# Kernel tuning notes

Hardware: AMD Instinct MI355X
Metric: run time of the kernel (lower is better)

Reference implementation:

```python
import jax, jax.numpy as jnp
import numpy as np

N_T, N_M, E, Q = 100000, 20000, 600000, 200000
F_IN, D, L = 256, 128, 2


def setup_inputs() -> dict:
    key = jax.random.key(0)
    ks = jax.random.split(key, 20)
    s = 1.0 / np.sqrt(D)
    inp = {
        "x_thesis": jax.random.normal(ks[0], (N_T, F_IN), jnp.float32),
        "mentor_node_id": jnp.arange(N_M, dtype=jnp.int64) if jax.config.jax_enable_x64 else jnp.arange(N_M, dtype=jnp.int32),
        "edge_src": jax.random.randint(ks[1], (E,), 0, N_T),
        "edge_dst": jax.random.randint(ks[2], (E,), 0, N_M),
        "eli_src": jax.random.randint(ks[3], (Q,), 0, N_T),
        "eli_dst": jax.random.randint(ks[4], (Q,), 0, N_M),
        # encoder params
        "thesis_lin_w": jax.random.normal(ks[5], (D, F_IN), jnp.float32) / np.sqrt(F_IN),
        "thesis_lin_b": jnp.zeros((D,), jnp.float32),
        "prof_emb": jax.random.normal(ks[6], (N_M, D), jnp.float32),
        # SAGEConv params per layer, per edge type (sup: thesis->mentor, rev: mentor->thesis)
        "W_nbr_sup": jax.random.normal(ks[7], (L, D, D), jnp.float32) * s,
        "W_root_sup": jax.random.normal(ks[8], (L, D, D), jnp.float32) * s,
        "b_sup": jnp.zeros((L, D), jnp.float32),
        "W_nbr_rev": jax.random.normal(ks[9], (L, D, D), jnp.float32) * s,
        "W_root_rev": jax.random.normal(ks[10], (L, D, D), jnp.float32) * s,
        "b_rev": jnp.zeros((L, D), jnp.float32),
        # classifier Linear(2*D -> 1)
        "cls_w": jax.random.normal(ks[11], (2 * D,), jnp.float32) * (1.0 / np.sqrt(2 * D)),
        "cls_b": jnp.zeros((), jnp.float32),
    }
    return inp


def reference(x_thesis, mentor_node_id, edge_src, edge_dst, eli_src, eli_dst,
              thesis_lin_w, thesis_lin_b, prof_emb,
              W_nbr_sup, W_root_sup, b_sup, W_nbr_rev, W_root_rev, b_rev,
              cls_w, cls_b):
    n_t = x_thesis.shape[0]
    n_m = prof_emb.shape[0]
    L_ = W_nbr_sup.shape[0]

    # node encoders
    h_t = x_thesis @ thesis_lin_w.T + thesis_lin_b          # [N_T, D]
    h_m = prof_emb[mentor_node_id]                          # [N_M, D]

    ones = jnp.ones(edge_src.shape[0], h_t.dtype)
    deg_m = jnp.maximum(jax.ops.segment_sum(ones, edge_dst, num_segments=n_m), 1.0)[:, None]
    deg_t = jnp.maximum(jax.ops.segment_sum(ones, edge_src, num_segments=n_t), 1.0)[:, None]

    for l in range(L_):
        # mean-aggregate thesis feats onto mentors (supervised_by edges)
        agg_m = jax.ops.segment_sum(h_t[edge_src], edge_dst, num_segments=n_m) / deg_m
        # mean-aggregate mentor feats onto theses (reverse edges)
        agg_t = jax.ops.segment_sum(h_m[edge_dst], edge_src, num_segments=n_t) / deg_t
        new_m = agg_m @ W_nbr_sup[l].T + h_m @ W_root_sup[l].T + b_sup[l]
        new_t = agg_t @ W_nbr_rev[l].T + h_t @ W_root_rev[l].T + b_rev[l]
        if l < L_ - 1:
            new_m = jax.nn.relu(new_m)
            new_t = jax.nn.relu(new_t)
        h_t, h_m = new_t, new_m

    # edge-level classifier: gather endpoints, concat, linear -> scalar per pair
    z = jnp.concatenate([h_t[eli_src], h_m[eli_dst]], axis=-1)  # [Q, 2D]
    return z @ cls_w + cls_b                                     # [Q]
```

## Files before the change

kernel.cpp:

```cpp
#include <hip/hip_runtime.h>
#include <cstdint>
#include <cstddef>

#define D 128
#define F_IN 256

typedef __attribute__((ext_vector_type(8))) short bf16x8;
typedef __attribute__((ext_vector_type(4))) float f32x4;

__device__ __forceinline__ unsigned short f2bs(float f) {
  unsigned int x = __builtin_bit_cast(unsigned int, f);
  x = x + 0x7fffu + ((x >> 16) & 1u);
  return (unsigned short)(x >> 16);
}
__device__ __forceinline__ unsigned pk2(float lo, float hi) {
  return (unsigned)f2bs(lo) | ((unsigned)f2bs(hi) << 16);
}
__device__ __forceinline__ float b2f(unsigned int lo16) {
  unsigned int x = lo16 << 16;
  return __builtin_bit_cast(float, x);
}
__device__ __forceinline__ void gl_lds16v(const void* g, void* l) {
  __builtin_amdgcn_global_load_lds(
      (__attribute__((address_space(1))) void*)g,
      (__attribute__((address_space(3))) void*)l, 16, 0, 0);
}
__device__ __forceinline__ uint4 pack8(float4 a, float4 b) {
  uint4 o;
  o.x = pk2(a.x, a.y); o.y = pk2(a.z, a.w);
  o.z = pk2(b.x, b.y); o.w = pk2(b.z, b.w);
  return o;
}


__global__ __launch_bounds__(256) void prep_k(
    const float* __restrict__ s0, unsigned short* __restrict__ d0, int n0,
    const float* __restrict__ s1, unsigned short* __restrict__ d1, int n1,
    const float* __restrict__ s2, unsigned short* __restrict__ d2, int n2,
    const float* __restrict__ s3, unsigned short* __restrict__ d3, int n3,
    const float* __restrict__ s4, unsigned short* __restrict__ d4, int n4,
    int nbC,
    const float* __restrict__ emb, const int* __restrict__ ids,
    unsigned short* __restrict__ hm, int NM, int nbG,
    const int* __restrict__ esrc, const int* __restrict__ edst,
    int* __restrict__ bktT, int* __restrict__ bktM,
    int E, int SHT, int SHM, int nbA)
{
  int bid = blockIdx.x;
  int tid = threadIdx.x;
  if (bid < nbC) {
    int j = bid * 256 + tid;
    const float* s; unsigned short* d;
    if (j < n0) { s = s0; d = d0; }
    else {
      j -= n0;
      if (j < n1) { s = s1; d = d1; }
      else {
        j -= n1;
        if (j < n2) { s = s2; d = d2; }
        else {
          j -= n2;
          if (j < n3) { s = s3; d = d3; }
          else { j -= n3; if (j >= n4) return; s = s4; d = d4; }
        }
      }
    }
    const float4* sp = (const float4*)(s + (size_t)j * 8);
    *(uint4*)(d + (size_t)j * 8) = pack8(sp[0], sp[1]);
    return;
  }
  bid -= nbC;
  if (bid < nbG) {
    int i = bid * 256 + tid;
    if (i >= NM * 16) return;
    int r = i >> 4, c = (i & 15) * 8;
    const float* s = emb + (size_t)ids[r] * D + c;
    *(uint4*)(hm + (size_t)r * D + c) = pack8(*(const float4*)s, *(const float4*)(s + 4));
    return;
  }
  bid -= nbG;
  __shared__ int sh[256];
  sh[tid] = 0;
  __syncthreads();
  int stride = nbA * 256;
  for (int e = bid * 256 + tid; e < E; e += stride) {
    atomicAdd(&sh[esrc[e] >> SHT], 1);
    atomicAdd(&sh[128 + (edst[e] >> SHM)], 1);
  }
  __syncthreads();
  if (tid < 128) { if (sh[tid]) atomicAdd(&bktT[tid], sh[tid]); }
  else { if (sh[tid]) atomicAdd(&bktM[tid - 128], sh[tid]); }
}


__global__ void a2_scan_k(const int* __restrict__ bktT, int* __restrict__ baseT, int* __restrict__ curT, int BT,
                          const int* __restrict__ bktM, int* __restrict__ baseM, int* __restrict__ curM, int BM) {
  __shared__ int sT[129], sM[129];
  int tid = threadIdx.x;
  if (tid < BT) sT[tid] = bktT[tid];
  if (tid < BM) sM[tid] = bktM[tid];
  __syncthreads();
  if (tid == 0) { int r = 0; for (int i = 0; i < BT; ++i) { int c = sT[i]; sT[i] = r; r += c; } sT[BT] = r; }
  if (tid == 1) { int r = 0; for (int i = 0; i < BM; ++i) { int c = sM[i]; sM[i] = r; r += c; } sM[BM] = r; }
  __syncthreads();
  if (tid <= BT) { baseT[tid] = sT[tid]; if (tid < BT) curT[tid] = sT[tid]; }
  if (tid <= BM) { baseM[tid] = sM[tid]; if (tid < BM) curM[tid] = sM[tid]; }
}


#define CH 4096

__global__ __launch_bounds__(256) void a3_part_k(
    const int* __restrict__ esrc, const int* __restrict__ edst,
    unsigned* __restrict__ partT, unsigned* __restrict__ partM,
    int* __restrict__ curT, int* __restrict__ curM,
    int E, int BT, int BM, int SHT, int SHM)
{
  __shared__ unsigned stT[CH], stM[CH];
  __shared__ int hT[128], lbT[128], lcT[128], gbT[128];
  __shared__ int hM[128], lbM[128], lcM[128], gbM[128];
  __shared__ int st2[256];
  int tid = threadIdx.x;
  int c0 = blockIdx.x * CH;
  int len = E - c0; if (len > CH) len = CH;

  if (tid < 128) { hT[tid] = 0; hM[tid] = 0; }
  __syncthreads();
  for (int i = tid; i < len; i += 256) {
    atomicAdd(&hT[esrc[c0 + i] >> SHT], 1);
    atomicAdd(&hM[edst[c0 + i] >> SHM], 1);
  }
  __syncthreads();
  int own = (tid < 128) ? hT[tid] : hM[tid - 128];
  st2[tid] = own;
  __syncthreads();
  for (int dd = 1; dd < 128; dd <<= 1) {
    int y = ((tid & 127) >= dd) ? st2[tid - dd] : 0;
    __syncthreads();
    st2[tid] += y;
    __syncthreads();
  }
  int excl = st2[tid] - own;
  if (tid < 128) { lbT[tid] = excl; lcT[tid] = excl; }
  else { lbM[tid - 128] = excl; lcM[tid - 128] = excl; }
  __syncthreads();
  if (tid < BT) { if (hT[tid]) gbT[tid] = atomicAdd(&curT[tid], hT[tid]); }
  if (tid >= 128 && tid - 128 < BM) { int m = tid - 128; if (hM[m]) gbM[m] = atomicAdd(&curM[m], hM[m]); }
  __syncthreads();
  for (int i = tid; i < len; i += 256) {
    unsigned s = (unsigned)esrc[c0 + i], dn = (unsigned)edst[c0 + i];
    int p = atomicAdd(&lcT[s >> SHT], 1);
    stT[p] = (s << 15) | dn;
    int q = atomicAdd(&lcM[dn >> SHM], 1);
    stM[q] = (dn << 17) | s;
  }
  __syncthreads();
  for (int b = 0; b < BT; ++b) {
    int cb = hT[b]; if (!cb) continue;
    int lb = lbT[b]; int gb = gbT[b];
    for (int i = tid; i < cb; i += 256) partT[gb + i] = stT[lb + i];
  }
  for (int b = 0; b < BM; ++b) {
    int cb = hM[b]; if (!cb) continue;
    int lb = lbM[b]; int gb = gbM[b];
    for (int i = tid; i < cb; i += 256) partM[gb + i] = stM[lb + i];
  }
}


#define BCAP 12288

__global__ __launch_bounds__(256) void b_csr_k(
    const unsigned* __restrict__ partT, const int* __restrict__ baseT,
    int* __restrict__ rowT, int* __restrict__ csrT, int NT, int BT, int SHT,
    const unsigned* __restrict__ partM, const int* __restrict__ baseM,
    int* __restrict__ rowM, int* __restrict__ csrM, int NM, int BM, int SHM, int E)
{
  __shared__ int cnt[1024];
  __shared__ int st[256];
  __shared__ unsigned stage[BCAP];

  const unsigned* part; const int* base; int* row; int* csr;
  int N, SH, KS; unsigned PM; int b; bool last;
  if ((int)blockIdx.x < BT) {
    part = partT; base = baseT; row = rowT; csr = csrT;
    N = NT; SH = SHT; KS = 15; PM = 0x7fffu; b = blockIdx.x; last = (b == BT - 1);
  } else {
    part = partM; base = baseM; row = rowM; csr = csrM;
    N = NM; SH = SHM; KS = 17; PM = 0x1ffffu; b = blockIdx.x - BT; last = (b == BM - 1);
  }
  int tid = threadIdx.x;
  int ebeg = base[b], eend = base[b + 1];
  int tot = eend - ebeg;
  int n0 = b << SH;
  int width = 1 << SH;
  int nw = N - n0; if (nw > width) nw = width;
  int seg = (width + 255) >> 8;

  for (int j = 0; j < seg; ++j) { int idx = tid * seg + j; if (idx < nw) cnt[idx] = 0; }
  __syncthreads();
  for (int i = tid; i < tot; i += 256) {
    int k = (int)(part[ebeg + i] >> KS) - n0;
    atomicAdd(&cnt[k], 1);
  }
  __syncthreads();
  int s = 0;
  for (int j = 0; j < seg; ++j) { int idx = tid * seg + j; if (idx < nw) s += cnt[idx]; }
  st[tid] = s;
  __syncthreads();
  for (int dd = 1; dd < 256; dd <<= 1) {
    int y = (tid >= dd) ? st[tid - dd] : 0;
    __syncthreads();
    st[tid] += y;
    __syncthreads();
  }
  int run = st[tid] - s;
  for (int j = 0; j < seg; ++j) {
    int idx = tid * seg + j;
    if (idx < nw) {
      int c = cnt[idx];
      row[n0 + idx] = ebeg + run;
      cnt[idx] = run;
      run += c;
    }
  }
  if (last && tid == 0) row[N] = E;
  __syncthreads();
  if (tot <= BCAP) {
    for (int i = tid; i < tot; i += 256) {
      unsigned p = part[ebeg + i];
      int k = (int)(p >> KS) - n0;
      int pos = atomicAdd(&cnt[k], 1);
      stage[pos] = p & PM;
    }
    __syncthreads();
    for (int i = tid; i < tot; i += 256) csr[ebeg + i] = (int)stage[i];
  } else {
    for (int i = tid; i < tot; i += 256) {
      unsigned p = part[ebeg + i];
      int k = (int)(p >> KS) - n0;
      int pos = atomicAdd(&cnt[k], 1);
      csr[ebeg + pos] = (int)(p & PM);
    }
  }
}


__global__ __launch_bounds__(256) void enc24_k(
    const float* __restrict__ A, const unsigned short* __restrict__ W,
    const float* __restrict__ bias, unsigned short* __restrict__ out, int M)
{
  __shared__ char smraw[24576];
  float* bufA = (float*)smraw;
  unsigned short* bufW = (unsigned short*)(smraw + 16384);
  const int tid = threadIdx.x;
  const int w = tid >> 6, l = tid & 63;
  const int wr = w >> 1, wc = w & 1;
  const int lr = l & 15, kg = l >> 4;
  const int row0 = blockIdx.x * 128;
  const int arow = l >> 3, au = l & 7;
  const int wrow = l >> 2, wu = l & 3;

  f32x4 acc[4][4] = {};

#pragma unroll 1
  for (int st = 0; st < F_IN / 32; ++st) {
    int k0 = st * 32;
#pragma unroll
    for (int q = 0; q < 4; ++q) {
      int r = w * 32 + q * 8 + arow;
      int gr = row0 + r; if (gr >= M) gr = M - 1;
      int gu = au ^ (r & 7);
      gl_lds16v(A + (size_t)gr * F_IN + k0 + gu * 4, bufA + r * 32 + au * 4);
    }
#pragma unroll
    for (int q = 0; q < 2; ++q) {
      int r = w * 32 + q * 16 + wrow;
      int gu = wu ^ ((r >> 1) & 3);
      gl_lds16v(W + (size_t)r * F_IN + k0 + gu * 8, bufW + r * 32 + wu * 8);
    }
    __syncthreads();
    bf16x8 aF[4], wF[4];
#pragma unroll
    for (int i = 0; i < 4; ++i) {
      int r = wr * 64 + i * 16 + lr;
      const float4* pa = (const float4*)(bufA + r * 32);
      float4 v0 = pa[(2 * kg) ^ (r & 7)];
      float4 v1 = pa[(2 * kg + 1) ^ (r & 7)];
      uint4 c = pack8(v0, v1);
      aF[i] = *(bf16x8*)&c;
    }
#pragma unroll
    for (int j = 0; j < 4; ++j) {
      int r = wc * 64 + j * 16 + lr;
      wF[j] = *(const bf16x8*)&bufW[r * 32 + ((kg ^ ((r >> 1) & 3)) * 8)];
    }
#pragma unroll
    for (int i = 0; i < 4; ++i)
#pragma unroll
      for (int j = 0; j < 4; ++j)
        acc[i][j] = __builtin_amdgcn_mfma_f32_16x16x32_bf16(aF[i], wF[j], acc[i][j], 0, 0, 0);
    __syncthreads();
  }

  float bn[4];
#pragma unroll
  for (int j = 0; j < 4; ++j) bn[j] = bias[wc * 64 + j * 16 + lr];
  unsigned short* stg = (unsigned short*)smraw;
#pragma unroll 1
  for (int half = 0; half < 2; ++half) {
    __syncthreads();
    if (wr == half) {
#pragma unroll
      for (int i = 0; i < 4; ++i)
#pragma unroll
        for (int j = 0; j < 4; ++j) {
          f32x4 v = acc[i][j];
#pragma unroll
          for (int r = 0; r < 4; ++r)
            stg[(i * 16 + kg * 4 + r) * 128 + wc * 64 + j * 16 + lr] = f2bs(v[r] + bn[j]);
        }
    }
    __syncthreads();
#pragma unroll
    for (int q = 0; q < 4; ++q) {
      int u = q * 256 + tid;
      int lrow = u >> 4;
      int cu = (u & 15) * 8;
      int gr = row0 + half * 64 + lrow;
      if (gr < M)
        *(uint4*)(out + (size_t)gr * D + cu) = *(const uint4*)&stg[lrow * 128 + cu];
    }
  }
}


__global__ __launch_bounds__(256) void aggregate3_k(
    const unsigned short* __restrict__ tabM, const int* __restrict__ rowpM,
    const int* __restrict__ idxM, unsigned short* __restrict__ outM, int nM, int nblkM,
    const unsigned short* __restrict__ tabT, const int* __restrict__ rowpT,
    const int* __restrict__ idxT, unsigned short* __restrict__ outT, int nT)
{
  const unsigned short* tab; const int* rowp; const int* idx;
  unsigned short* outp; int n, nodeb;
  if ((int)blockIdx.x < nblkM) {
    tab = tabM; rowp = rowpM; idx = idxM; outp = outM; n = nM;
    nodeb = blockIdx.x * 8;
  } else {
    tab = tabT; rowp = rowpT; idx = idxT; outp = outT; n = nT;
    nodeb = (blockIdx.x - nblkM) * 8;
  }
  const int tid = threadIdx.x;
  const int l = tid & 63;
  const int sub = l >> 5;
  const int half = (l >> 4) & 1;
  const int l16 = l & 15;
  const int node = nodeb + (tid >> 6) * 2 + sub;
  const int nodeC = node < n ? node : n - 1;
  int b = rowp[nodeC];
  int e = rowp[nodeC + 1];
  if (node >= n) e = b;
  const int deg = e - b;
  int nb = (deg + 15) >> 4;
  int onb = __shfl_xor(nb, 32, 64);
  int trip = nb > onb ? nb : onb;
  const unsigned short* tl = tab + l16 * 8;

  float a0 = 0.f, a1 = 0.f, a2 = 0.f, a3 = 0.f;
  float a4 = 0.f, a5 = 0.f, a6 = 0.f, a7 = 0.f;
  for (int t = 0; t < trip; ++t) {
    int base = b + t * 16 + half;
    int pp[8]; bool ok[8];
#pragma unroll
    for (int u = 0; u < 8; ++u) {
      int p = base + 2 * u;
      ok[u] = p < e;
      pp[u] = ok[u] ? idx[p] : 0;
    }
    uint4 vv[8];
#pragma unroll
    for (int u = 0; u < 8; ++u) {
      uint4 z; z.x = 0u; z.y = 0u; z.z = 0u; z.w = 0u;
      vv[u] = z;
      if (ok[u]) vv[u] = *(const uint4*)(tl + (size_t)pp[u] * D);
    }
#pragma unroll
    for (int u = 0; u < 8; ++u) {
      a0 += b2f(vv[u].x & 0xffffu); a1 += b2f(vv[u].x >> 16);
      a2 += b2f(vv[u].y & 0xffffu); a3 += b2f(vv[u].y >> 16);
      a4 += b2f(vv[u].z & 0xffffu); a5 += b2f(vv[u].z >> 16);
      a6 += b2f(vv[u].w & 0xffffu); a7 += b2f(vv[u].w >> 16);
    }
  }
  a0 += __shfl_xor(a0, 16, 64);
  a1 += __shfl_xor(a1, 16, 64);
  a2 += __shfl_xor(a2, 16, 64);
  a3 += __shfl_xor(a3, 16, 64);
  a4 += __shfl_xor(a4, 16, 64);
  a5 += __shfl_xor(a5, 16, 64);
  a6 += __shfl_xor(a6, 16, 64);
  a7 += __shfl_xor(a7, 16, 64);
  if (node < n && half == 0) {
    float inv = 1.0f / (float)(deg > 1 ? deg : 1);
    uint4 o;
    o.x = pk2(a0 * inv, a1 * inv);
    o.y = pk2(a2 * inv, a3 * inv);
    o.z = pk2(a4 * inv, a5 * inv);
    o.w = pk2(a6 * inv, a7 * inv);
    *(uint4*)(outp + (size_t)node * D + l16 * 8) = o;
  }
}


template<bool RELU>
__device__ __forceinline__ void gemm_body(
    const unsigned short* __restrict__ Aop, const unsigned short* __restrict__ WA,
    const unsigned short* __restrict__ Bop, const unsigned short* __restrict__ WB,
    const float* __restrict__ bias, unsigned short* __restrict__ out, int M,
    int blk, char* smraw)
{
  unsigned short* bufA0 = (unsigned short*)smraw;
  unsigned short* bufW0 = (unsigned short*)(smraw + 16384);
  const int tid = threadIdx.x;
  const int w = tid >> 6, l = tid & 63;
  const int wr = w >> 1, wc = w & 1;
  const int lr = l & 15, kg = l >> 4;
  const int row0 = blk * 128;
  const int srow = l >> 2;
  const int su = l & 3;

  f32x4 acc[4][4] = {};

  auto stage = [&](int st, int bsel) {
    const unsigned short* Ap = (st < 4) ? Aop : Bop;
    const unsigned short* Wp = (st < 4) ? WA : WB;
    int k0 = (st & 3) * 32;
    unsigned short* bA = bufA0 + bsel * 4096;
    unsigned short* bW = bufW0 + bsel * 4096;
#pragma unroll
    for (int q = 0; q < 2; ++q) {
      int r = w * 32 + q * 16 + srow;
      int gr = row0 + r; if (gr >= M) gr = M - 1;
      int gu = su ^ ((r >> 1) & 3);
      gl_lds16v(Ap + (size_t)gr * D + k0 + gu * 8, bA + (w * 32 + q * 16) * 32 + l * 8);
      gl_lds16v(Wp + (size_t)r * D + k0 + gu * 8, bW + (w * 32 + q * 16) * 32 + l * 8);
    }
  };

  stage(0, 0);
#pragma unroll 1
  for (int st = 0; st < 8; ++st) {
    if (st < 7) {
      stage(st + 1, (st + 1) & 1);
      __builtin_amdgcn_sched_barrier(0);
      asm volatile("s_waitcnt vmcnt(4)" ::: "memory");
    } else {
      __builtin_amdgcn_sched_barrier(0);
      asm volatile("s_waitcnt vmcnt(0)" ::: "memory");
    }
    __builtin_amdgcn_s_barrier();
    __builtin_amdgcn_sched_barrier(0);
    const unsigned short* bA = bufA0 + (st & 1) * 4096;
    const unsigned short* bW = bufW0 + (st & 1) * 4096;
    bf16x8 aF[4], bF[4];
#pragma unroll
    for (int i = 0; i < 4; ++i) {
      int r = wr * 64 + i * 16 + lr;
      aF[i] = *(const bf16x8*)&bA[r * 32 + ((kg ^ ((r >> 1) & 3)) * 8)];
    }
#pragma unroll
    for (int j = 0; j < 4; ++j) {
      int r = wc * 64 + j * 16 + lr;
      bF[j] = *(const bf16x8*)&bW[r * 32 + ((kg ^ ((r >> 1) & 3)) * 8)];
    }
#pragma unroll
    for (int i = 0; i < 4; ++i)
#pragma unroll
      for (int j = 0; j < 4; ++j)
        acc[i][j] = __builtin_amdgcn_mfma_f32_16x16x32_bf16(aF[i], bF[j], acc[i][j], 0, 0, 0);
    __builtin_amdgcn_sched_barrier(0);
    __builtin_amdgcn_s_barrier();
  }

  __syncthreads();
  float bn[4];
#pragma unroll
  for (int j = 0; j < 4; ++j) bn[j] = bias[wc * 64 + j * 16 + lr];
  unsigned short* ow = (unsigned short*)smraw + w * 4096;
#pragma unroll
  for (int i = 0; i < 4; ++i)
#pragma unroll
    for (int j = 0; j < 4; ++j) {
      f32x4 v = acc[i][j];
#pragma unroll
      for (int r = 0; r < 4; ++r) {
        float x = v[r] + bn[j];
        if (RELU) x = fmaxf(x, 0.f);
        ow[(i * 16 + kg * 4 + r) * 64 + j * 16 + lr] = f2bs(x);
      }
    }
  __syncthreads();
#pragma unroll
  for (int q = 0; q < 8; ++q) {
    int u = q * 64 + l;
    int lrow = u >> 3;
    int cu = (u & 7) * 8;
    int gr = row0 + wr * 64 + lrow;
    if (gr < M)
      *(uint4*)(out + (size_t)gr * D + wc * 64 + cu) = *(const uint4*)&ow[lrow * 64 + cu];
  }
}

template<bool RELU>
__global__ __launch_bounds__(256) void gemm_pair_k(
    const unsigned short* __restrict__ Am, const unsigned short* __restrict__ WAm,
    const unsigned short* __restrict__ Bm, const unsigned short* __restrict__ WBm,
    const float* __restrict__ biasm, unsigned short* __restrict__ outm, int Mm, int nbm,
    const unsigned short* __restrict__ At, const unsigned short* __restrict__ WAt,
    const unsigned short* __restrict__ Bt, const unsigned short* __restrict__ WBt,
    const float* __restrict__ biast, unsigned short* __restrict__ outt, int Mt)
{
  __shared__ char smraw[32768];
  if ((int)blockIdx.x < nbm)
    gemm_body<RELU>(Am, WAm, Bm, WBm, biasm, outm, Mm, blockIdx.x, smraw);
  else
    gemm_body<RELU>(At, WAt, Bt, WBt, biast, outt, Mt, blockIdx.x - nbm, smraw);
}


__global__ __launch_bounds__(256) void classify_k(
    const unsigned short* __restrict__ ht, const unsigned short* __restrict__ hm,
    const int* __restrict__ qs, const int* __restrict__ qd,
    const float* __restrict__ w, const float* __restrict__ bptr,
    float* __restrict__ out, int Q)
{
  int g = blockIdx.x * 8 + (threadIdx.x >> 5);
  if (g >= Q) return;
  int l = threadIdx.x & 31;
  const unsigned short* src = (l < 16)
      ? ht + (size_t)qs[g] * D + l * 8
      : hm + (size_t)qd[g] * D + (l - 16) * 8;
  uint4 v = *(const uint4*)src;
  const float* wp = w + l * 8;
  float acc = 0.f;
  acc += b2f(v.x & 0xffffu) * wp[0];
  acc += b2f(v.x >> 16)     * wp[1];
  acc += b2f(v.y & 0xffffu) * wp[2];
  acc += b2f(v.y >> 16)     * wp[3];
  acc += b2f(v.z & 0xffffu) * wp[4];
  acc += b2f(v.z >> 16)     * wp[5];
  acc += b2f(v.w & 0xffffu) * wp[6];
  acc += b2f(v.w >> 16)     * wp[7];
#pragma unroll
  for (int m = 16; m >= 1; m >>= 1) acc += __shfl_xor(acc, m, 64);
  if (l == 0) out[g] = acc + bptr[0];
}


extern "C" void kernel_launch(void* const* d_in, const int* in_sizes, int n_in,
                              void* d_out, int out_size, void* d_ws, size_t ws_size,
                              hipStream_t stream)
{
  const float* x_thesis = (const float*)d_in[0];
  const int*   mentor_id = (const int*)d_in[1];
  const int*   esrc = (const int*)d_in[2];
  const int*   edst = (const int*)d_in[3];
  const int*   qsrc = (const int*)d_in[4];
  const int*   qdst = (const int*)d_in[5];
  const float* lin_w = (const float*)d_in[6];
  const float* lin_b = (const float*)d_in[7];
  const float* prof  = (const float*)d_in[8];
  const float* Wn_sup = (const float*)d_in[9];
  const float* Wr_sup = (const float*)d_in[10];
  const float* b_sup  = (const float*)d_in[11];
  const float* Wn_rev = (const float*)d_in[12];
  const float* Wr_rev = (const float*)d_in[13];
  const float* b_rev  = (const float*)d_in[14];
  const float* cls_w  = (const float*)d_in[15];
  const float* cls_b  = (const float*)d_in[16];

  const int NT = in_sizes[0] / F_IN;
  const int NM = in_sizes[1];
  const int E  = in_sizes[2];
  const int Q  = in_sizes[4];
  const int L  = in_sizes[11] / D;

  int SHT = 0; while ((((NT - 1) >> SHT) + 1) > 128) ++SHT;
  int SHM = 0; while ((((NM - 1) >> SHM) + 1) > 128) ++SHM;
  const int BT = ((NT - 1) >> SHT) + 1;
  const int BM = ((NM - 1) >> SHM) + 1;

  char* wsb = (char*)d_ws;
  size_t off = 0;
  auto alloc = [&](size_t bytes) {
    void* p = wsb + off;
    off = (off + bytes + 255) & ~(size_t)255;
    return p;
  };
  unsigned short* h_t   = (unsigned short*)alloc((size_t)NT * D * 2);
  unsigned short* a_t   = (unsigned short*)alloc((size_t)NT * D * 2);
  unsigned short* h_m   = (unsigned short*)alloc((size_t)NM * D * 2);
  unsigned short* a_m   = (unsigned short*)alloc((size_t)NM * D * 2);
  unsigned short* linw_bf = (unsigned short*)alloc((size_t)D * F_IN * 2);
  unsigned short* wns_bf  = (unsigned short*)alloc((size_t)L * D * D * 2);
  unsigned short* wrs_bf  = (unsigned short*)alloc((size_t)L * D * D * 2);
  unsigned short* wnr_bf  = (unsigned short*)alloc((size_t)L * D * D * 2);
  unsigned short* wrr_bf  = (unsigned short*)alloc((size_t)L * D * D * 2);
  int* row_t = (int*)alloc(((size_t)NT + 1) * 4);
  int* row_m = (int*)alloc(((size_t)NM + 1) * 4);
  int* csr_t = (int*)alloc((size_t)E * 4);
  int* csr_m = (int*)alloc((size_t)E * 4);
  unsigned* partT = (unsigned*)alloc((size_t)E * 4);
  unsigned* partM = (unsigned*)alloc((size_t)E * 4);
  size_t bkt_off = off;
  int* bktT  = (int*)alloc(128 * 4);
  int* bktM  = (int*)alloc(128 * 4);
  size_t bkt_end = off;
  int* baseT = (int*)alloc(129 * 4);
  int* baseM = (int*)alloc(129 * 4);
  int* curT  = (int*)alloc(128 * 4);
  int* curM  = (int*)alloc(128 * 4);
  (void)n_in; (void)out_size; (void)ws_size;

  (void)hipMemsetAsync(wsb + bkt_off, 0, bkt_end - bkt_off, stream);

  {
    int n0 = D * F_IN / 8, nw = L * D * D / 8;
    int totc = n0 + 4 * nw;
    int nbC = (totc + 255) / 256;
    int nbG = (NM * 16 + 255) / 256;
    int nbA = 256;
    prep_k<<<nbC + nbG + nbA, 256, 0, stream>>>(
        lin_w, linw_bf, n0, Wn_sup, wns_bf, nw, Wr_sup, wrs_bf, nw,
        Wn_rev, wnr_bf, nw, Wr_rev, wrr_bf, nw, nbC,
        prof, mentor_id, h_m, NM, nbG,
        esrc, edst, bktT, bktM, E, SHT, SHM, nbA);
  }
  a2_scan_k<<<1, 256, 0, stream>>>(bktT, baseT, curT, BT, bktM, baseM, curM, BM);
  a3_part_k<<<(E + CH - 1) / CH, 256, 0, stream>>>(
      esrc, edst, partT, partM, curT, curM, E, BT, BM, SHT, SHM);
  b_csr_k<<<BT + BM, 256, 0, stream>>>(
      partT, baseT, row_t, csr_t, NT, BT, SHT,
      partM, baseM, row_m, csr_m, NM, BM, SHM, E);

  enc24_k<<<(NT + 127) / 128, 256, 0, stream>>>(x_thesis, linw_bf, lin_b, h_t, NT);

  int agg_nbm = (NM + 7) / 8, agg_nbt = (NT + 7) / 8;
  int gem_nbm = (NM + 127) / 128, gem_nbt = (NT + 127) / 128;
  for (int l = 0; l < L; ++l) {
    aggregate3_k<<<agg_nbm + agg_nbt, 256, 0, stream>>>(
        h_t, row_m, csr_m, a_m, NM, agg_nbm,
        h_m, row_t, csr_t, a_t, NT);

    const unsigned short* wns = wns_bf + (size_t)l * D * D;
    const unsigned short* wrs = wrs_bf + (size_t)l * D * D;
    const unsigned short* wnr = wnr_bf + (size_t)l * D * D;
    const unsigned short* wrr = wrr_bf + (size_t)l * D * D;
    const float* bs = b_sup + (size_t)l * D;
    const float* br = b_rev + (size_t)l * D;
    if (l < L - 1) {
      gemm_pair_k<true><<<gem_nbm + gem_nbt, 256, 0, stream>>>(
          a_m, wns, h_m, wrs, bs, a_m, NM, gem_nbm,
          a_t, wnr, h_t, wrr, br, a_t, NT);
    } else {
      gemm_pair_k<false><<<gem_nbm + gem_nbt, 256, 0, stream>>>(
          a_m, wns, h_m, wrs, bs, a_m, NM, gem_nbm,
          a_t, wnr, h_t, wrr, br, a_t, NT);
    }
    unsigned short* tmp;
    tmp = h_t; h_t = a_t; a_t = tmp;
    tmp = h_m; h_m = a_m; a_m = tmp;
  }

  classify_k<<<(Q + 7) / 8, 256, 0, stream>>>(h_t, h_m, qsrc, qdst, cls_w, cls_b,
                                              (float*)d_out, Q);
}
```

Baseline: 271.0 us.

## Fold classifier into last-layer GEMM and co-schedule aggregation with GEMMs

The last-layer GEMMs now compute each node's dot product with its half of the classifier weight in the epilogue and write a single scalar per node. The final classifier then becomes two scalar gathers per query instead of two 256-byte row gathers. The launch schedule is also reordered so independent aggregation blocks share a launch with the encoder or a GEMM, cutting the kernel count and the serial gaps between stages. The cost is LDS float atomics in the epilogue and extra buffers so the reordered stages don't overwrite inputs still in use.

```diff
diff --git a/kernel.cpp b/kernel.cpp
--- a/kernel.cpp
+++ b/kernel.cpp
@@ -246,116 +246,17 @@
 }
 
 
-__global__ __launch_bounds__(256) void enc24_k(
-    const float* __restrict__ A, const unsigned short* __restrict__ W,
-    const float* __restrict__ bias, unsigned short* __restrict__ out, int M)
-{
-  __shared__ char smraw[24576];
-  float* bufA = (float*)smraw;
-  unsigned short* bufW = (unsigned short*)(smraw + 16384);
-  const int tid = threadIdx.x;
-  const int w = tid >> 6, l = tid & 63;
-  const int wr = w >> 1, wc = w & 1;
-  const int lr = l & 15, kg = l >> 4;
-  const int row0 = blockIdx.x * 128;
-  const int arow = l >> 3, au = l & 7;
-  const int wrow = l >> 2, wu = l & 3;
-
-  f32x4 acc[4][4] = {};
-
-#pragma unroll 1
-  for (int st = 0; st < F_IN / 32; ++st) {
-    int k0 = st * 32;
-#pragma unroll
-    for (int q = 0; q < 4; ++q) {
-      int r = w * 32 + q * 8 + arow;
-      int gr = row0 + r; if (gr >= M) gr = M - 1;
-      int gu = au ^ (r & 7);
-      gl_lds16v(A + (size_t)gr * F_IN + k0 + gu * 4, bufA + r * 32 + au * 4);
-    }
-#pragma unroll
-    for (int q = 0; q < 2; ++q) {
-      int r = w * 32 + q * 16 + wrow;
-      int gu = wu ^ ((r >> 1) & 3);
-      gl_lds16v(W + (size_t)r * F_IN + k0 + gu * 8, bufW + r * 32 + wu * 8);
-    }
-    __syncthreads();
-    bf16x8 aF[4], wF[4];
-#pragma unroll
-    for (int i = 0; i < 4; ++i) {
-      int r = wr * 64 + i * 16 + lr;
-      const float4* pa = (const float4*)(bufA + r * 32);
-      float4 v0 = pa[(2 * kg) ^ (r & 7)];
-      float4 v1 = pa[(2 * kg + 1) ^ (r & 7)];
-      uint4 c = pack8(v0, v1);
-      aF[i] = *(bf16x8*)&c;
-    }
-#pragma unroll
-    for (int j = 0; j < 4; ++j) {
-      int r = wc * 64 + j * 16 + lr;
-      wF[j] = *(const bf16x8*)&bufW[r * 32 + ((kg ^ ((r >> 1) & 3)) * 8)];
-    }
-#pragma unroll
-    for (int i = 0; i < 4; ++i)
-#pragma unroll
-      for (int j = 0; j < 4; ++j)
-        acc[i][j] = __builtin_amdgcn_mfma_f32_16x16x32_bf16(aF[i], wF[j], acc[i][j], 0, 0, 0);
-    __syncthreads();
-  }
-
-  float bn[4];
-#pragma unroll
-  for (int j = 0; j < 4; ++j) bn[j] = bias[wc * 64 + j * 16 + lr];
-  unsigned short* stg = (unsigned short*)smraw;
-#pragma unroll 1
-  for (int half = 0; half < 2; ++half) {
-    __syncthreads();
-    if (wr == half) {
-#pragma unroll
-      for (int i = 0; i < 4; ++i)
-#pragma unroll
-        for (int j = 0; j < 4; ++j) {
-          f32x4 v = acc[i][j];
-#pragma unroll
-          for (int r = 0; r < 4; ++r)
-            stg[(i * 16 + kg * 4 + r) * 128 + wc * 64 + j * 16 + lr] = f2bs(v[r] + bn[j]);
-        }
-    }
-    __syncthreads();
-#pragma unroll
-    for (int q = 0; q < 4; ++q) {
-      int u = q * 256 + tid;
-      int lrow = u >> 4;
-      int cu = (u & 15) * 8;
-      int gr = row0 + half * 64 + lrow;
-      if (gr < M)
-        *(uint4*)(out + (size_t)gr * D + cu) = *(const uint4*)&stg[lrow * 128 + cu];
-    }
-  }
-}
-
-
-__global__ __launch_bounds__(256) void aggregate3_k(
-    const unsigned short* __restrict__ tabM, const int* __restrict__ rowpM,
-    const int* __restrict__ idxM, unsigned short* __restrict__ outM, int nM, int nblkM,
-    const unsigned short* __restrict__ tabT, const int* __restrict__ rowpT,
-    const int* __restrict__ idxT, unsigned short* __restrict__ outT, int nT)
-{
-  const unsigned short* tab; const int* rowp; const int* idx;
-  unsigned short* outp; int n, nodeb;
-  if ((int)blockIdx.x < nblkM) {
-    tab = tabM; rowp = rowpM; idx = idxM; outp = outM; n = nM;
-    nodeb = blockIdx.x * 8;
-  } else {
-    tab = tabT; rowp = rowpT; idx = idxT; outp = outT; n = nT;
-    nodeb = (blockIdx.x - nblkM) * 8;
-  }
+__device__ __forceinline__ void agg_body(
+    const unsigned short* __restrict__ tab, const int* __restrict__ rowp,
+    const int* __restrict__ idx, unsigned short* __restrict__ outp,
+    int n, int blk)
+{
   const int tid = threadIdx.x;
   const int l = tid & 63;
   const int sub = l >> 5;
   const int half = (l >> 4) & 1;
   const int l16 = l & 15;
-  const int node = nodeb + (tid >> 6) * 2 + sub;
+  const int node = blk * 8 + (tid >> 6) * 2 + sub;
   const int nodeC = node < n ? node : n - 1;
   int b = rowp[nodeC];
   int e = rowp[nodeC + 1];
@@ -411,13 +312,101 @@
   }
 }
 
-
-template<bool RELU>
+__device__ __forceinline__ void enc_body(
+    const float* __restrict__ A, const unsigned short* __restrict__ W,
+    const float* __restrict__ bias, unsigned short* __restrict__ out, int M,
+    int blk, char* smraw)
+{
+  float* bufA = (float*)smraw;
+  unsigned short* bufW = (unsigned short*)(smraw + 16384);
+  const int tid = threadIdx.x;
+  const int w = tid >> 6, l = tid & 63;
+  const int wr = w >> 1, wc = w & 1;
+  const int lr = l & 15, kg = l >> 4;
+  const int row0 = blk * 128;
+  const int arow = l >> 3, au = l & 7;
+  const int wrow = l >> 2, wu = l & 3;
+
+  f32x4 acc[4][4] = {};
+
+#pragma unroll 1
+  for (int st = 0; st < F_IN / 32; ++st) {
+    int k0 = st * 32;
+#pragma unroll
+    for (int q = 0; q < 4; ++q) {
+      int r = w * 32 + q * 8 + arow;
+      int gr = row0 + r; if (gr >= M) gr = M - 1;
+      int gu = au ^ (r & 7);
+      gl_lds16v(A + (size_t)gr * F_IN + k0 + gu * 4, bufA + r * 32 + au * 4);
+    }
+#pragma unroll
+    for (int q = 0; q < 2; ++q) {
+      int r = w * 32 + q * 16 + wrow;
+      int gu = wu ^ ((r >> 1) & 3);
+      gl_lds16v(W + (size_t)r * F_IN + k0 + gu * 8, bufW + r * 32 + wu * 8);
+    }
+    __syncthreads();
+    bf16x8 aF[4], wF[4];
+#pragma unroll
+    for (int i = 0; i < 4; ++i) {
+      int r = wr * 64 + i * 16 + lr;
+      const float4* pa = (const float4*)(bufA + r * 32);
+      float4 v0 = pa[(2 * kg) ^ (r & 7)];
+      float4 v1 = pa[(2 * kg + 1) ^ (r & 7)];
+      uint4 c = pack8(v0, v1);
+      aF[i] = *(bf16x8*)&c;
+    }
+#pragma unroll
+    for (int j = 0; j < 4; ++j) {
+      int r = wc * 64 + j * 16 + lr;
+      wF[j] = *(const bf16x8*)&bufW[r * 32 + ((kg ^ ((r >> 1) & 3)) * 8)];
+    }
+#pragma unroll
+    for (int i = 0; i < 4; ++i)
+#pragma unroll
+      for (int j = 0; j < 4; ++j)
+        acc[i][j] = __builtin_amdgcn_mfma_f32_16x16x32_bf16(aF[i], wF[j], acc[i][j], 0, 0, 0);
+    __syncthreads();
+  }
+
+  float bn[4];
+#pragma unroll
+  for (int j = 0; j < 4; ++j) bn[j] = bias[wc * 64 + j * 16 + lr];
+  unsigned short* stg = (unsigned short*)smraw;
+#pragma unroll 1
+  for (int half = 0; half < 2; ++half) {
+    __syncthreads();
+    if (wr == half) {
+#pragma unroll
+      for (int i = 0; i < 4; ++i)
+#pragma unroll
+        for (int j = 0; j < 4; ++j) {
+          f32x4 v = acc[i][j];
+#pragma unroll
+          for (int r = 0; r < 4; ++r)
+            stg[(i * 16 + kg * 4 + r) * 128 + wc * 64 + j * 16 + lr] = f2bs(v[r] + bn[j]);
+        }
+    }
+    __syncthreads();
+#pragma unroll
+    for (int q = 0; q < 4; ++q) {
+      int u = q * 256 + tid;
+      int lrow = u >> 4;
+      int cu = (u & 15) * 8;
+      int gr = row0 + half * 64 + lrow;
+      if (gr < M)
+        *(uint4*)(out + (size_t)gr * D + cu) = *(const uint4*)&stg[lrow * 128 + cu];
+    }
+  }
+}
+
+template<bool RELU, bool LAST>
 __device__ __forceinline__ void gemm_body(
     const unsigned short* __restrict__ Aop, const unsigned short* __restrict__ WA,
     const unsigned short* __restrict__ Bop, const unsigned short* __restrict__ WB,
-    const float* __restrict__ bias, unsigned short* __restrict__ out, int M,
-    int blk, char* smraw)
+    const float* __restrict__ bias, unsigned short* __restrict__ out,
+    float* __restrict__ stout, const float* __restrict__ wcls,
+    int M, int blk, char* smraw)
 {
   unsigned short* bufA0 = (unsigned short*)smraw;
   unsigned short* bufW0 = (unsigned short*)(smraw + 16384);
@@ -486,6 +475,39 @@
   float bn[4];
 #pragma unroll
   for (int j = 0; j < 4; ++j) bn[j] = bias[wc * 64 + j * 16 + lr];
+
+  if (LAST) {
+    float* rowsum = (float*)smraw;
+    if (tid < 128) rowsum[tid] = 0.f;
+    __syncthreads();
+    float wv[4];
+#pragma unroll
+    for (int j = 0; j < 4; ++j) wv[j] = wcls[wc * 64 + j * 16 + lr];
+#pragma unroll
+    for (int i = 0; i < 4; ++i) {
+      float part[4] = {0.f, 0.f, 0.f, 0.f};
+#pragma unroll
+      for (int j = 0; j < 4; ++j) {
+        f32x4 v = acc[i][j];
+#pragma unroll
+        for (int r = 0; r < 4; ++r) {
+          float x = v[r] + bn[j];
+          if (RELU) x = fmaxf(x, 0.f);
+          part[r] += x * wv[j];
+        }
+      }
+#pragma unroll
+      for (int r = 0; r < 4; ++r)
+        atomicAdd(&rowsum[wr * 64 + i * 16 + kg * 4 + r], part[r]);
+    }
+    __syncthreads();
+    if (tid < 128) {
+      int gr = row0 + tid;
+      if (gr < M) stout[gr] = rowsum[tid];
+    }
+    return;
+  }
+
   unsigned short* ow = (unsigned short*)smraw + w * 4096;
 #pragma unroll
   for (int i = 0; i < 4; ++i)
@@ -511,49 +533,44 @@
   }
 }
 
-template<bool RELU>
-__global__ __launch_bounds__(256) void gemm_pair_k(
-    const unsigned short* __restrict__ Am, const unsigned short* __restrict__ WAm,
-    const unsigned short* __restrict__ Bm, const unsigned short* __restrict__ WBm,
-    const float* __restrict__ biasm, unsigned short* __restrict__ outm, int Mm, int nbm,
-    const unsigned short* __restrict__ At, const unsigned short* __restrict__ WAt,
-    const unsigned short* __restrict__ Bt, const unsigned short* __restrict__ WBt,
-    const float* __restrict__ biast, unsigned short* __restrict__ outt, int Mt)
+
+__global__ __launch_bounds__(256) void enc_agg_k(
+    const float* __restrict__ A, const unsigned short* __restrict__ W,
+    const float* __restrict__ bias, unsigned short* __restrict__ ht, int M, int nbEnc,
+    const unsigned short* __restrict__ tab, const int* __restrict__ rowp,
+    const int* __restrict__ idx, unsigned short* __restrict__ outa, int na)
+{
+  __shared__ char smraw[24576];
+  if ((int)blockIdx.x < nbEnc)
+    enc_body(A, W, bias, ht, M, blockIdx.x, smraw);
+  else
+    agg_body(tab, rowp, idx, outa, na, blockIdx.x - nbEnc);
+}
+
+template<bool RELU, bool LAST>
+__global__ __launch_bounds__(256) void gemm_agg_k(
+    const unsigned short* __restrict__ Ag, const unsigned short* __restrict__ WAg,
+    const unsigned short* __restrict__ Bg, const unsigned short* __restrict__ WBg,
+    const float* __restrict__ biasg, unsigned short* __restrict__ outg,
+    float* __restrict__ stoutg, const float* __restrict__ wclsg, int Mg, int nbG,
+    const unsigned short* __restrict__ tab, const int* __restrict__ rowp,
+    const int* __restrict__ idx, unsigned short* __restrict__ outa, int na)
 {
   __shared__ char smraw[32768];
-  if ((int)blockIdx.x < nbm)
-    gemm_body<RELU>(Am, WAm, Bm, WBm, biasm, outm, Mm, blockIdx.x, smraw);
+  if ((int)blockIdx.x < nbG)
+    gemm_body<RELU, LAST>(Ag, WAg, Bg, WBg, biasg, outg, stoutg, wclsg, Mg, blockIdx.x, smraw);
   else
-    gemm_body<RELU>(At, WAt, Bt, WBt, biast, outt, Mt, blockIdx.x - nbm, smraw);
-}
-
-
-__global__ __launch_bounds__(256) void classify_k(
-    const unsigned short* __restrict__ ht, const unsigned short* __restrict__ hm,
+    agg_body(tab, rowp, idx, outa, na, blockIdx.x - nbG);
+}
+
+
+__global__ __launch_bounds__(256) void classify2_k(
+    const float* __restrict__ st, const float* __restrict__ sm,
     const int* __restrict__ qs, const int* __restrict__ qd,
-    const float* __restrict__ w, const float* __restrict__ bptr,
-    float* __restrict__ out, int Q)
-{
-  int g = blockIdx.x * 8 + (threadIdx.x >> 5);
-  if (g >= Q) return;
-  int l = threadIdx.x & 31;
-  const unsigned short* src = (l < 16)
-      ? ht + (size_t)qs[g] * D + l * 8
-      : hm + (size_t)qd[g] * D + (l - 16) * 8;
-  uint4 v = *(const uint4*)src;
-  const float* wp = w + l * 8;
-  float acc = 0.f;
-  acc += b2f(v.x & 0xffffu) * wp[0];
-  acc += b2f(v.x >> 16)     * wp[1];
-  acc += b2f(v.y & 0xffffu) * wp[2];
-  acc += b2f(v.y >> 16)     * wp[3];
-  acc += b2f(v.z & 0xffffu) * wp[4];
-  acc += b2f(v.z >> 16)     * wp[5];
-  acc += b2f(v.w & 0xffffu) * wp[6];
-  acc += b2f(v.w >> 16)     * wp[7];
-#pragma unroll
-  for (int m = 16; m >= 1; m >>= 1) acc += __shfl_xor(acc, m, 64);
-  if (l == 0) out[g] = acc + bptr[0];
+    const float* __restrict__ bptr, float* __restrict__ out, int Q)
+{
+  int g = blockIdx.x * 256 + threadIdx.x;
+  if (g < Q) out[g] = st[qs[g]] + sm[qd[g]] + bptr[0];
 }
 
 
@@ -597,10 +614,15 @@
     off = (off + bytes + 255) & ~(size_t)255;
     return p;
   };
-  unsigned short* h_t   = (unsigned short*)alloc((size_t)NT * D * 2);
-  unsigned short* a_t   = (unsigned short*)alloc((size_t)NT * D * 2);
-  unsigned short* h_m   = (unsigned short*)alloc((size_t)NM * D * 2);
-  unsigned short* a_m   = (unsigned short*)alloc((size_t)NM * D * 2);
+  unsigned short* h_t0  = (unsigned short*)alloc((size_t)NT * D * 2);
+  unsigned short* a_t0  = (unsigned short*)alloc((size_t)NT * D * 2);
+  unsigned short* h_t1  = (unsigned short*)alloc((size_t)NT * D * 2);
+  unsigned short* h_m0  = (unsigned short*)alloc((size_t)NM * D * 2);
+  unsigned short* a_m0  = (unsigned short*)alloc((size_t)NM * D * 2);
+  unsigned short* h_m1  = (unsigned short*)alloc((size_t)NM * D * 2);
+  unsigned short* a_m1  = (unsigned short*)alloc((size_t)NM * D * 2);
+  float* stT = (float*)alloc((size_t)NT * 4);
+  float* smM = (float*)alloc((size_t)NM * 4);
   unsigned short* linw_bf = (unsigned short*)alloc((size_t)D * F_IN * 2);
   unsigned short* wns_bf  = (unsigned short*)alloc((size_t)L * D * D * 2);
   unsigned short* wrs_bf  = (unsigned short*)alloc((size_t)L * D * D * 2);
@@ -633,7 +655,7 @@
     prep_k<<<nbC + nbG + nbA, 256, 0, stream>>>(
         lin_w, linw_bf, n0, Wn_sup, wns_bf, nw, Wr_sup, wrs_bf, nw,
         Wn_rev, wnr_bf, nw, Wr_rev, wrr_bf, nw, nbC,
-        prof, mentor_id, h_m, NM, nbG,
+        prof, mentor_id, h_m0, NM, nbG,
         esrc, edst, bktT, bktM, E, SHT, SHM, nbA);
   }
   a2_scan_k<<<1, 256, 0, stream>>>(bktT, baseT, curT, BT, bktM, baseM, curM, BM);
@@ -643,35 +665,74 @@
       partT, baseT, row_t, csr_t, NT, BT, SHT,
       partM, baseM, row_m, csr_m, NM, BM, SHM, E);
 
-  enc24_k<<<(NT + 127) / 128, 256, 0, stream>>>(x_thesis, linw_bf, lin_b, h_t, NT);
-
-  int agg_nbm = (NM + 7) / 8, agg_nbt = (NT + 7) / 8;
-  int gem_nbm = (NM + 127) / 128, gem_nbt = (NT + 127) / 128;
-  for (int l = 0; l < L; ++l) {
-    aggregate3_k<<<agg_nbm + agg_nbt, 256, 0, stream>>>(
-        h_t, row_m, csr_m, a_m, NM, agg_nbm,
-        h_m, row_t, csr_t, a_t, NT);
-
-    const unsigned short* wns = wns_bf + (size_t)l * D * D;
-    const unsigned short* wrs = wrs_bf + (size_t)l * D * D;
-    const unsigned short* wnr = wnr_bf + (size_t)l * D * D;
-    const unsigned short* wrr = wrr_bf + (size_t)l * D * D;
-    const float* bs = b_sup + (size_t)l * D;
-    const float* br = b_rev + (size_t)l * D;
-    if (l < L - 1) {
-      gemm_pair_k<true><<<gem_nbm + gem_nbt, 256, 0, stream>>>(
-          a_m, wns, h_m, wrs, bs, a_m, NM, gem_nbm,
-          a_t, wnr, h_t, wrr, br, a_t, NT);
-    } else {
-      gemm_pair_k<false><<<gem_nbm + gem_nbt, 256, 0, stream>>>(
-          a_m, wns, h_m, wrs, bs, a_m, NM, gem_nbm,
-          a_t, wnr, h_t, wrr, br, a_t, NT);
-    }
-    unsigned short* tmp;
-    tmp = h_t; h_t = a_t; a_t = tmp;
-    tmp = h_m; h_m = a_m; a_m = tmp;
-  }
-
-  classify_k<<<(Q + 7) / 8, 256, 0, stream>>>(h_t, h_m, qsrc, qdst, cls_w, cls_b,
-                                              (float*)d_out, Q);
-}
+  const int aggT_nb = (NT + 7) / 8, aggM_nb = (NM + 7) / 8;
+  const int gemT_nb = (NT + 127) / 128, gemM_nb = (NM + 127) / 128;
+  const int nbEnc = (NT + 127) / 128;
+
+  if (L == 2) {
+    const unsigned short *wns0 = wns_bf, *wns1 = wns_bf + (size_t)D * D;
+    const unsigned short *wrs0 = wrs_bf, *wrs1 = wrs_bf + (size_t)D * D;
+    const unsigned short *wnr0 = wnr_bf, *wnr1 = wnr_bf + (size_t)D * D;
+    const unsigned short *wrr0 = wrr_bf, *wrr1 = wrr_bf + (size_t)D * D;
+    const float *bs0 = b_sup, *bs1 = b_sup + D;
+    const float *br0 = b_rev, *br1 = b_rev + D;
+
+    enc_agg_k<<<nbEnc + aggT_nb, 256, 0, stream>>>(
+        x_thesis, linw_bf, lin_b, h_t0, NT, nbEnc,
+        h_m0, row_t, csr_t, a_t0, NT);
+    gemm_agg_k<true, false><<<gemT_nb + aggM_nb, 256, 0, stream>>>(
+        a_t0, wnr0, h_t0, wrr0, br0, h_t1, nullptr, nullptr, NT, gemT_nb,
+        h_t0, row_m, csr_m, a_m0, NM);
+    gemm_agg_k<true, false><<<gemM_nb + aggM_nb, 256, 0, stream>>>(
+        a_m0, wns0, h_m0, wrs0, bs0, h_m1, nullptr, nullptr, NM, gemM_nb,
+        h_t1, row_m, csr_m, a_m1, NM);
+    gemm_agg_k<false, true><<<gemM_nb + aggT_nb, 256, 0, stream>>>(
+        a_m1, wns1, h_m1, wrs1, bs1, nullptr, smM, cls_w + D, NM, gemM_nb,
+        h_m1, row_t, csr_t, a_t0, NT);
+    gemm_agg_k<false, true><<<gemT_nb, 256, 0, stream>>>(
+        a_t0, wnr1, h_t1, wrr1, br1, nullptr, stT, cls_w, NT, gemT_nb,
+        nullptr, nullptr, nullptr, nullptr, 0);
+    classify2_k<<<(Q + 255) / 256, 256, 0, stream>>>(
+        stT, smM, qsrc, qdst, cls_b, (float*)d_out, Q);
+  } else {
+    enc_agg_k<<<nbEnc, 256, 0, stream>>>(
+        x_thesis, linw_bf, lin_b, h_t0, NT, nbEnc,
+        nullptr, nullptr, nullptr, nullptr, 0);
+    unsigned short *h_t = h_t0, *a_t = a_t0, *h_m = h_m0, *a_m = a_m0;
+    for (int l = 0; l < L; ++l) {
+      bool lastl = (l == L - 1);
+      const unsigned short* wns = wns_bf + (size_t)l * D * D;
+      const unsigned short* wrs = wrs_bf + (size_t)l * D * D;
+      const unsigned short* wnr = wnr_bf + (size_t)l * D * D;
+      const unsigned short* wrr = wrr_bf + (size_t)l * D * D;
+      const float* bs = b_sup + (size_t)l * D;
+      const float* br = b_rev + (size_t)l * D;
+      gemm_agg_k<true, false><<<aggM_nb, 256, 0, stream>>>(
+          nullptr, nullptr, nullptr, nullptr, nullptr, nullptr, nullptr, nullptr, 0, 0,
+          h_t, row_m, csr_m, a_m, NM);
+      gemm_agg_k<true, false><<<aggT_nb, 256, 0, stream>>>(
+          nullptr, nullptr, nullptr, nullptr, nullptr, nullptr, nullptr, nullptr, 0, 0,
+          h_m, row_t, csr_t, a_t, NT);
+      if (!lastl) {
+        gemm_agg_k<true, false><<<gemM_nb, 256, 0, stream>>>(
+            a_m, wns, h_m, wrs, bs, a_m, nullptr, nullptr, NM, gemM_nb,
+            nullptr, nullptr, nullptr, nullptr, 0);
+        gemm_agg_k<true, false><<<gemT_nb, 256, 0, stream>>>(
+            a_t, wnr, h_t, wrr, br, a_t, nullptr, nullptr, NT, gemT_nb,
+            nullptr, nullptr, nullptr, nullptr, 0);
+        unsigned short* tmp;
+        tmp = h_t; h_t = a_t; a_t = tmp;
+        tmp = h_m; h_m = a_m; a_m = tmp;
+      } else {
+        gemm_agg_k<false, true><<<gemM_nb, 256, 0, stream>>>(
+            a_m, wns, h_m, wrs, bs, nullptr, smM, cls_w + D, NM, gemM_nb,
+            nullptr, nullptr, nullptr, nullptr, 0);
+        gemm_agg_k<false, true><<<gemT_nb, 256, 0, stream>>>(
+            a_t, wnr, h_t, wrr, br, nullptr, stT, cls_w, NT, gemT_nb,
+            nullptr, nullptr, nullptr, nullptr, 0);
+      }
+    }
+    classify2_k<<<(Q + 255) / 256, 256, 0, stream>>>(
+        stT, smM, qsrc, qdst, cls_b, (float*)d_out, Q);
+  }
+}
```

Result: slower. 345.3 us (+27.4%).
